# Kernel optimization log

Measured on AMD Instinct MI355X. Metric: run time of the kernel, lower is better.

## Reference

```python
import jax, jax.numpy as jnp
import numpy as np

B, T, F, H = 2048, 512, 64, 16


def setup_inputs() -> dict:
    key = jax.random.key(0)
    ks = jax.random.split(key, 10)
    s = 0.05  # small init so relu-activated LSTM state stays bounded over 512 steps
    return {
        "x": jax.random.normal(ks[0], (B, T, F), dtype=jnp.float32),
        "Wx": jax.random.normal(ks[1], (F, 4 * H), dtype=jnp.float32) * s,
        "Wh": jax.random.normal(ks[2], (H, 4 * H), dtype=jnp.float32) * s,
        "b": jnp.zeros((4 * H,), dtype=jnp.float32),
        "W2": jax.random.normal(ks[3], (H, 8), dtype=jnp.float32) * 0.3,
        "b2": jnp.zeros((8,), dtype=jnp.float32),
        "W3": jax.random.normal(ks[4], (8, 4), dtype=jnp.float32) * 0.3,
        "b3": jnp.zeros((4,), dtype=jnp.float32),
        "Wo": jax.random.normal(ks[5], (4, 1), dtype=jnp.float32) * 0.3,
        "bo": jnp.zeros((1,), dtype=jnp.float32),
    }


def reference(x, Wx, Wh, b, W2, b2, W3, b3, Wo, bo):
    # Keras LSTM, gate order [i, f, c(g), o]; recurrent_activation=sigmoid,
    # activation=relu (applied to candidate g AND to cell state in h = o*relu(c)).
    # Precompute input projections for all timesteps, scan only the recurrence.
    xz = jnp.einsum('btf,fg->btg', x, Wx) + b  # [B, T, 4H]
    h0 = jnp.zeros((x.shape[0], H), dtype=x.dtype)
    c0 = jnp.zeros((x.shape[0], H), dtype=x.dtype)

    def step(carry, xz_t):
        h, c = carry
        z = xz_t + h @ Wh  # [B, 4H]
        i = jax.nn.sigmoid(z[:, 0 * H:1 * H])
        f = jax.nn.sigmoid(z[:, 1 * H:2 * H])
        g = jax.nn.relu(z[:, 2 * H:3 * H])
        o = jax.nn.sigmoid(z[:, 3 * H:4 * H])
        c_new = f * c + i * g
        h_new = o * jax.nn.relu(c_new)
        return (h_new, c_new), None

    (h_T, _), _ = jax.lax.scan(step, (h0, c0), jnp.swapaxes(xz, 0, 1))
    # Dropout layers are identity at inference (training=False).
    x2 = jax.nn.relu(h_T @ W2 + b2)
    x3 = jax.nn.relu(x2 @ W3 + b3)
    return jax.nn.sigmoid(x3 @ Wo + bo)  # [B, 1]
```

## Files before the change

### kernel.cpp

```cpp
#include <hip/hip_runtime.h>
#include <stdint.h>

#define Bdim 2048
#define Tdim 512
#define NTILE 32

typedef __attribute__((ext_vector_type(8))) short bf16x8;
typedef __attribute__((ext_vector_type(4))) float f32x4;

union U32x4 { uint32_t u[4]; bf16x8 v; };

__device__ __forceinline__ uint16_t f2bf(float f) {
    union { float f; uint32_t u; } v; v.f = f;
    uint32_t r = v.u + 0x7fffu + ((v.u >> 16) & 1u);
    return (uint16_t)(r >> 16);
}
__device__ __forceinline__ float sigmoidf(float z) {
    return __builtin_amdgcn_rcpf(1.0f + __expf(-z));
}
__device__ __forceinline__ float fast_exp2(float x) {
#if __has_builtin(__builtin_amdgcn_exp2f)
    return __builtin_amdgcn_exp2f(x);
#else
    return exp2f(x);
#endif
}

#define RORI(M, dst, src)                                                     \
    dst = __builtin_amdgcn_update_dpp((src), (src), 0x120 | (M), 0xF, 0xF, 0)

#define FMAC_ROR(M, ACC)                                                      \
    asm("v_fmac_f32 %0, %1, %2 row_ror:" #M " row_mask:0xf bank_mask:0xf"     \
        : "+v"(ACC) : "v"(h), "v"(w[M]))

__global__ __launch_bounds__(64, 2) void lstm_fused(
    const float* __restrict__ x, const float* __restrict__ Wx,
    const float* __restrict__ bias, const float* __restrict__ Wh,
    const float* __restrict__ W2, const float* __restrict__ b2,
    const float* __restrict__ W3, const float* __restrict__ b3,
    const float* __restrict__ Wo, const float* __restrict__ bo,
    float* __restrict__ out)
{
    __shared__ __align__(16) float zbuf[2048];
    __shared__ float hs[16];

    const int lane = threadIdx.x;
    const int u    = lane & 15;
    const int quad = lane >> 4;
    const int col  = quad * 16 + u;
    const int b    = blockIdx.x;
    const float NL2E = -1.4426950408889634f;
    const float sg   = (quad == 2) ? 1.0f : NL2E;

    float w[16];
    w[0] = Wh[(size_t)u * 64 + col] * sg;
#define WL(M) { int ii_; RORI(M, ii_, u); w[M] = Wh[(size_t)ii_ * 64 + col] * sg; }
    WL(1)  WL(2)  WL(3)  WL(4)  WL(5)  WL(6)  WL(7)
    WL(8)  WL(9)  WL(10) WL(11) WL(12) WL(13) WL(14) WL(15)
#undef WL

    const int adr_i = (u +  0) * 4;
    const int adr_f = (u + 16) * 4;
    const int adr_g = (u + 32) * 4;
    const int adr_o = (u + 48) * 4;

    bf16x8 wxf[4][2];
    float bv[4];
    #pragma unroll
    for (int nt = 0; nt < 4; ++nt) {
        const float s = (nt == 2) ? 1.0f : NL2E;
        #pragma unroll
        for (int kc = 0; kc < 2; ++kc)
            #pragma unroll
            for (int e = 0; e < 8; ++e)
                wxf[nt][kc][e] = (short)f2bf(
                    Wx[(size_t)(kc * 32 + quad * 8 + e) * 64 + nt * 16 + u] * s);
        bv[nt] = bias[nt * 16 + u] * s;
    }

    f32x4 xa0[4], xa1[4];
    auto xload = [&](int tile, f32x4 (&xs)[4]) {
        const float* p = x + ((size_t)b * Tdim + tile * 16 + u) * 64 + quad * 8;
        xs[0] = *(const f32x4*)(p);
        xs[1] = *(const f32x4*)(p + 4);
        xs[2] = *(const f32x4*)(p + 32);
        xs[3] = *(const f32x4*)(p + 36);
    };

    auto proj = [&](const f32x4 (&xs)[4], int buf) {
        U32x4 af[2];
        #pragma unroll
        for (int kc = 0; kc < 2; ++kc) {
            asm("v_cvt_pk_bf16_f32 %0, %1, %2" : "=v"(af[kc].u[0]) : "v"(xs[2*kc][0]),   "v"(xs[2*kc][1]));
            asm("v_cvt_pk_bf16_f32 %0, %1, %2" : "=v"(af[kc].u[1]) : "v"(xs[2*kc][2]),   "v"(xs[2*kc][3]));
            asm("v_cvt_pk_bf16_f32 %0, %1, %2" : "=v"(af[kc].u[2]) : "v"(xs[2*kc+1][0]), "v"(xs[2*kc+1][1]));
            asm("v_cvt_pk_bf16_f32 %0, %1, %2" : "=v"(af[kc].u[3]) : "v"(xs[2*kc+1][2]), "v"(xs[2*kc+1][3]));
        }
        float* zb = zbuf + buf * 1024 + quad * 256 + u * 4;
        #pragma unroll
        for (int nt = 0; nt < 4; ++nt) {
            f32x4 a = {bv[nt], bv[nt], bv[nt], bv[nt]};
            a = __builtin_amdgcn_mfma_f32_16x16x32_bf16(af[0].v, wxf[nt][0], a, 0, 0, 0);
            a = __builtin_amdgcn_mfma_f32_16x16x32_bf16(af[1].v, wxf[nt][1], a, 0, 0, 0);
            *(f32x4*)(zb + nt * 64) = a;
        }
    };

    xload(0, xa0);
    proj(xa0, 0);
    xload(1, xa1);

    float c = 0.f, h = 0.f;
    f32x4 zgA = *(const f32x4*)(zbuf + col * 4);
    f32x4 zgB;

    const bool isrelu = (quad == 2);

    auto scan_tile = [&](int n) {
        const float* curp = zbuf + (n & 1) * 1024 + col * 4;
        const float* othp = zbuf + ((n & 1) ^ 1) * 1024 + col * 4;
        #pragma unroll
        for (int t = 0; t < 16; ++t) {
            const int gl = t >> 2;
            if ((t & 3) == 0) {
                const float* zp = (gl < 3) ? (curp + (gl + 1) * 256) : othp;
                f32x4 zv = *(const f32x4*)zp;
                if (gl & 1) zgA = zv; else zgB = zv;
            }
            const float zval = (gl & 1) ? zgB[t & 3] : zgA[t & 3];

            asm volatile("s_nop 1" : "+v"(h));

            float acc0 = fmaf(h, w[0], zval);
            float acc1 = 0.f;
            FMAC_ROR(1,  acc1); FMAC_ROR(2,  acc0); FMAC_ROR(3,  acc1);
            FMAC_ROR(4,  acc0); FMAC_ROR(5,  acc1); FMAC_ROR(6,  acc0);
            FMAC_ROR(7,  acc1); FMAC_ROR(8,  acc0); FMAC_ROR(9,  acc1);
            FMAC_ROR(10, acc0); FMAC_ROR(11, acc1); FMAC_ROR(12, acc0);
            FMAC_ROR(13, acc1); FMAC_ROR(14, acc0); FMAC_ROR(15, acc1);
            const float zacc = acc0 + acc1;

            const float sig = __builtin_amdgcn_rcpf(1.0f + fast_exp2(zacc));
            const float a   = isrelu ? fmaxf(zacc, 0.0f) : sig;

            const int ia = __float_as_int(a);
            const float gi = __int_as_float(__builtin_amdgcn_ds_bpermute(adr_i, ia));
            const float gf = __int_as_float(__builtin_amdgcn_ds_bpermute(adr_f, ia));
            const float gG = __int_as_float(__builtin_amdgcn_ds_bpermute(adr_g, ia));
            const float go = __int_as_float(__builtin_amdgcn_ds_bpermute(adr_o, ia));

            c = fmaf(gf, c, gi * gG);
            h = go * fmaxf(c, 0.0f);
        }
    };

    #pragma unroll 1
    for (int nn = 0; nn < NTILE / 2; ++nn) {
        {
            const int n = 2 * nn;
            if (n + 2 < NTILE) xload(n + 2, xa0);
            proj(xa1, 1);
            scan_tile(n);
        }
        {
            const int n = 2 * nn + 1;
            if (n + 2 < NTILE) xload(n + 2, xa1);
            if (n + 1 < NTILE) proj(xa0, 0);
            scan_tile(n);
        }
    }

    if (lane < 16) hs[lane] = h;
    if (lane == 0) {
        float x2[8];
        #pragma unroll
        for (int k = 0; k < 8; ++k) {
            float s = b2[k];
            #pragma unroll
            for (int q = 0; q < 16; ++q) s = fmaf(hs[q], W2[(size_t)q * 8 + k], s);
            x2[k] = fmaxf(s, 0.f);
        }
        float x3[4];
        #pragma unroll
        for (int m = 0; m < 4; ++m) {
            float s = b3[m];
            #pragma unroll
            for (int k = 0; k < 8; ++k) s = fmaf(x2[k], W3[(size_t)k * 4 + m], s);
            x3[m] = fmaxf(s, 0.f);
        }
        float s = bo[0];
        #pragma unroll
        for (int m = 0; m < 4; ++m) s = fmaf(x3[m], Wo[m], s);
        out[b] = sigmoidf(s);
    }
}

extern "C" void kernel_launch(void* const* d_in, const int* in_sizes, int n_in,
                              void* d_out, int out_size, void* d_ws, size_t ws_size,
                              hipStream_t stream) {
    const float* x  = (const float*)d_in[0];
    const float* Wx = (const float*)d_in[1];
    const float* Wh = (const float*)d_in[2];
    const float* bb = (const float*)d_in[3];
    const float* W2 = (const float*)d_in[4];
    const float* b2 = (const float*)d_in[5];
    const float* W3 = (const float*)d_in[6];
    const float* b3 = (const float*)d_in[7];
    const float* Wo = (const float*)d_in[8];
    const float* bo = (const float*)d_in[9];

    lstm_fused<<<Bdim, 64, 0, stream>>>(x, Wx, bb, Wh, W2, b2, W3, b3,
                                        Wo, bo, (float*)d_out);
}
```

Measured before the change: 381.2 us.

## Pack four batch rows per wavefront and compute all gates per lane

Each 64-lane wavefront now handles four batch rows (one per 16-lane row group) instead of one, with each lane computing all four gate dot products for its hidden unit. This removes the four ds_bpermute gate exchanges per step, and the grid shrinks to a quarter of the blocks. The cost is four times the DPP FMAs per step, 64 recurrent weights per lane, larger LDS buffers and occupancy hint 1, so the serial per-step latency grows while the work per lane is used better.

```diff
diff --git a/kernel.cpp b/kernel.cpp
--- a/kernel.cpp
+++ b/kernel.cpp
@@ -4,6 +4,7 @@
 #define Bdim 2048
 #define Tdim 512
 #define NTILE 32
+#define ROWS 4
 
 typedef __attribute__((ext_vector_type(8))) short bf16x8;
 typedef __attribute__((ext_vector_type(4))) float f32x4;
@@ -29,11 +30,11 @@
 #define RORI(M, dst, src)                                                     \
     dst = __builtin_amdgcn_update_dpp((src), (src), 0x120 | (M), 0xF, 0xF, 0)
 
-#define FMAC_ROR(M, ACC)                                                      \
+#define FMAC_ROR(M, ACC, H, W)                                                \
     asm("v_fmac_f32 %0, %1, %2 row_ror:" #M " row_mask:0xf bank_mask:0xf"     \
-        : "+v"(ACC) : "v"(h), "v"(w[M]))
-
-__global__ __launch_bounds__(64, 2) void lstm_fused(
+        : "+v"(ACC) : "v"(H), "v"(W))
+
+__global__ __launch_bounds__(64, 1) void lstm_fused(
     const float* __restrict__ x, const float* __restrict__ Wx,
     const float* __restrict__ bias, const float* __restrict__ Wh,
     const float* __restrict__ W2, const float* __restrict__ b2,
@@ -41,28 +42,29 @@
     const float* __restrict__ Wo, const float* __restrict__ bo,
     float* __restrict__ out)
 {
-    __shared__ __align__(16) float zbuf[2048];
-    __shared__ float hs[16];
+    __shared__ __align__(16) float zbuf[8192];
+    __shared__ float hb[64];
 
     const int lane = threadIdx.x;
     const int u    = lane & 15;
     const int quad = lane >> 4;
-    const int col  = quad * 16 + u;
-    const int b    = blockIdx.x;
+    const int b0   = blockIdx.x * ROWS;
     const float NL2E = -1.4426950408889634f;
-    const float sg   = (quad == 2) ? 1.0f : NL2E;
-
-    float w[16];
-    w[0] = Wh[(size_t)u * 64 + col] * sg;
-#define WL(M) { int ii_; RORI(M, ii_, u); w[M] = Wh[(size_t)ii_ * 64 + col] * sg; }
-    WL(1)  WL(2)  WL(3)  WL(4)  WL(5)  WL(6)  WL(7)
-    WL(8)  WL(9)  WL(10) WL(11) WL(12) WL(13) WL(14) WL(15)
-#undef WL
-
-    const int adr_i = (u +  0) * 4;
-    const int adr_f = (u + 16) * 4;
-    const int adr_g = (u + 32) * 4;
-    const int adr_o = (u + 48) * 4;
+
+    int idx[16];
+    idx[0] = u;
+#define PR(M) RORI(M, idx[M], u);
+    PR(1)  PR(2)  PR(3)  PR(4)  PR(5)  PR(6)  PR(7)
+    PR(8)  PR(9)  PR(10) PR(11) PR(12) PR(13) PR(14) PR(15)
+#undef PR
+    float w[4][16];
+    #pragma unroll
+    for (int g = 0; g < 4; ++g) {
+        const float s = (g == 2) ? 1.0f : NL2E;
+        #pragma unroll
+        for (int k = 0; k < 16; ++k)
+            w[g][k] = Wh[(size_t)idx[k] * 64 + g * 16 + u] * s;
+    }
 
     bf16x8 wxf[4][2];
     float bv[4];
@@ -78,106 +80,108 @@
         bv[nt] = bias[nt * 16 + u] * s;
     }
 
-    f32x4 xa0[4], xa1[4];
-    auto xload = [&](int tile, f32x4 (&xs)[4]) {
-        const float* p = x + ((size_t)b * Tdim + tile * 16 + u) * 64 + quad * 8;
-        xs[0] = *(const f32x4*)(p);
-        xs[1] = *(const f32x4*)(p + 4);
-        xs[2] = *(const f32x4*)(p + 32);
-        xs[3] = *(const f32x4*)(p + 36);
+    f32x4 xa[ROWS][4];
+    auto xload = [&](int tile) {
+        #pragma unroll
+        for (int rs = 0; rs < ROWS; ++rs) {
+            const float* p = x + ((size_t)(b0 + rs) * Tdim + tile * 16 + u) * 64
+                               + quad * 8;
+            xa[rs][0] = *(const f32x4*)(p);
+            xa[rs][1] = *(const f32x4*)(p + 4);
+            xa[rs][2] = *(const f32x4*)(p + 32);
+            xa[rs][3] = *(const f32x4*)(p + 36);
+        }
     };
 
-    auto proj = [&](const f32x4 (&xs)[4], int buf) {
-        U32x4 af[2];
-        #pragma unroll
-        for (int kc = 0; kc < 2; ++kc) {
-            asm("v_cvt_pk_bf16_f32 %0, %1, %2" : "=v"(af[kc].u[0]) : "v"(xs[2*kc][0]),   "v"(xs[2*kc][1]));
-            asm("v_cvt_pk_bf16_f32 %0, %1, %2" : "=v"(af[kc].u[1]) : "v"(xs[2*kc][2]),   "v"(xs[2*kc][3]));
-            asm("v_cvt_pk_bf16_f32 %0, %1, %2" : "=v"(af[kc].u[2]) : "v"(xs[2*kc+1][0]), "v"(xs[2*kc+1][1]));
-            asm("v_cvt_pk_bf16_f32 %0, %1, %2" : "=v"(af[kc].u[3]) : "v"(xs[2*kc+1][2]), "v"(xs[2*kc+1][3]));
-        }
-        float* zb = zbuf + buf * 1024 + quad * 256 + u * 4;
-        #pragma unroll
-        for (int nt = 0; nt < 4; ++nt) {
-            f32x4 a = {bv[nt], bv[nt], bv[nt], bv[nt]};
-            a = __builtin_amdgcn_mfma_f32_16x16x32_bf16(af[0].v, wxf[nt][0], a, 0, 0, 0);
-            a = __builtin_amdgcn_mfma_f32_16x16x32_bf16(af[1].v, wxf[nt][1], a, 0, 0, 0);
-            *(f32x4*)(zb + nt * 64) = a;
+    auto proj = [&](int buf) {
+        #pragma unroll
+        for (int rs = 0; rs < ROWS; ++rs) {
+            U32x4 af0, af1;
+            asm("v_cvt_pk_bf16_f32 %0, %1, %2" : "=v"(af0.u[0]) : "v"(xa[rs][0][0]), "v"(xa[rs][0][1]));
+            asm("v_cvt_pk_bf16_f32 %0, %1, %2" : "=v"(af0.u[1]) : "v"(xa[rs][0][2]), "v"(xa[rs][0][3]));
+            asm("v_cvt_pk_bf16_f32 %0, %1, %2" : "=v"(af0.u[2]) : "v"(xa[rs][1][0]), "v"(xa[rs][1][1]));
+            asm("v_cvt_pk_bf16_f32 %0, %1, %2" : "=v"(af0.u[3]) : "v"(xa[rs][1][2]), "v"(xa[rs][1][3]));
+            asm("v_cvt_pk_bf16_f32 %0, %1, %2" : "=v"(af1.u[0]) : "v"(xa[rs][2][0]), "v"(xa[rs][2][1]));
+            asm("v_cvt_pk_bf16_f32 %0, %1, %2" : "=v"(af1.u[1]) : "v"(xa[rs][2][2]), "v"(xa[rs][2][3]));
+            asm("v_cvt_pk_bf16_f32 %0, %1, %2" : "=v"(af1.u[2]) : "v"(xa[rs][3][0]), "v"(xa[rs][3][1]));
+            asm("v_cvt_pk_bf16_f32 %0, %1, %2" : "=v"(af1.u[3]) : "v"(xa[rs][3][2]), "v"(xa[rs][3][3]));
+            f32x4 a0 = {bv[0], bv[0], bv[0], bv[0]};
+            f32x4 a1 = {bv[1], bv[1], bv[1], bv[1]};
+            f32x4 a2 = {bv[2], bv[2], bv[2], bv[2]};
+            f32x4 a3 = {bv[3], bv[3], bv[3], bv[3]};
+            a0 = __builtin_amdgcn_mfma_f32_16x16x32_bf16(af0.v, wxf[0][0], a0, 0, 0, 0);
+            a0 = __builtin_amdgcn_mfma_f32_16x16x32_bf16(af1.v, wxf[0][1], a0, 0, 0, 0);
+            a1 = __builtin_amdgcn_mfma_f32_16x16x32_bf16(af0.v, wxf[1][0], a1, 0, 0, 0);
+            a1 = __builtin_amdgcn_mfma_f32_16x16x32_bf16(af1.v, wxf[1][1], a1, 0, 0, 0);
+            a2 = __builtin_amdgcn_mfma_f32_16x16x32_bf16(af0.v, wxf[2][0], a2, 0, 0, 0);
+            a2 = __builtin_amdgcn_mfma_f32_16x16x32_bf16(af1.v, wxf[2][1], a2, 0, 0, 0);
+            a3 = __builtin_amdgcn_mfma_f32_16x16x32_bf16(af0.v, wxf[3][0], a3, 0, 0, 0);
+            a3 = __builtin_amdgcn_mfma_f32_16x16x32_bf16(af1.v, wxf[3][1], a3, 0, 0, 0);
+            float* zb = zbuf + buf * 4096 + quad * 1024 + rs * 64 + u * 4;
+            #pragma unroll
+            for (int r = 0; r < 4; ++r) {
+                float4 w4;
+                w4.x = a0[r]; w4.y = a1[r]; w4.z = a2[r]; w4.w = a3[r];
+                *(float4*)(zb + r * 256) = w4;
+            }
         }
     };
 
-    xload(0, xa0);
-    proj(xa0, 0);
-    xload(1, xa1);
+    xload(0);
+    proj(0);
+    xload(1);
 
     float c = 0.f, h = 0.f;
-    f32x4 zgA = *(const f32x4*)(zbuf + col * 4);
-    f32x4 zgB;
-
-    const bool isrelu = (quad == 2);
+    f32x4 zc = *(const f32x4*)(zbuf + quad * 64 + u * 4);
 
     auto scan_tile = [&](int n) {
-        const float* curp = zbuf + (n & 1) * 1024 + col * 4;
-        const float* othp = zbuf + ((n & 1) ^ 1) * 1024 + col * 4;
+        const float* zp = zbuf + (n & 1) * 4096 + quad * 64 + u * 4;
+        const float* zo = zbuf + ((n & 1) ^ 1) * 4096 + quad * 64 + u * 4;
         #pragma unroll
         for (int t = 0; t < 16; ++t) {
-            const int gl = t >> 2;
-            if ((t & 3) == 0) {
-                const float* zp = (gl < 3) ? (curp + (gl + 1) * 256) : othp;
-                f32x4 zv = *(const f32x4*)zp;
-                if (gl & 1) zgA = zv; else zgB = zv;
-            }
-            const float zval = (gl & 1) ? zgB[t & 3] : zgA[t & 3];
+            const float* zq = (t < 15) ? (zp + (t + 1) * 256) : zo;
+            f32x4 zn = *(const f32x4*)zq;
 
             asm volatile("s_nop 1" : "+v"(h));
 
-            float acc0 = fmaf(h, w[0], zval);
-            float acc1 = 0.f;
-            FMAC_ROR(1,  acc1); FMAC_ROR(2,  acc0); FMAC_ROR(3,  acc1);
-            FMAC_ROR(4,  acc0); FMAC_ROR(5,  acc1); FMAC_ROR(6,  acc0);
-            FMAC_ROR(7,  acc1); FMAC_ROR(8,  acc0); FMAC_ROR(9,  acc1);
-            FMAC_ROR(10, acc0); FMAC_ROR(11, acc1); FMAC_ROR(12, acc0);
-            FMAC_ROR(13, acc1); FMAC_ROR(14, acc0); FMAC_ROR(15, acc1);
-            const float zacc = acc0 + acc1;
-
-            const float sig = __builtin_amdgcn_rcpf(1.0f + fast_exp2(zacc));
-            const float a   = isrelu ? fmaxf(zacc, 0.0f) : sig;
-
-            const int ia = __float_as_int(a);
-            const float gi = __int_as_float(__builtin_amdgcn_ds_bpermute(adr_i, ia));
-            const float gf = __int_as_float(__builtin_amdgcn_ds_bpermute(adr_f, ia));
-            const float gG = __int_as_float(__builtin_amdgcn_ds_bpermute(adr_g, ia));
-            const float go = __int_as_float(__builtin_amdgcn_ds_bpermute(adr_o, ia));
-
-            c = fmaf(gf, c, gi * gG);
-            h = go * fmaxf(c, 0.0f);
+            float ai = fmaf(h, w[0][0], zc[0]);
+            float afv = fmaf(h, w[1][0], zc[1]);
+            float ag = fmaf(h, w[2][0], zc[2]);
+            float ao = fmaf(h, w[3][0], zc[3]);
+#define DOT4(M) FMAC_ROR(M, ai, h, w[0][M]); FMAC_ROR(M, afv, h, w[1][M]);    \
+                FMAC_ROR(M, ag, h, w[2][M]); FMAC_ROR(M, ao, h, w[3][M]);
+            DOT4(1)  DOT4(2)  DOT4(3)  DOT4(4)  DOT4(5)  DOT4(6)  DOT4(7)
+            DOT4(8)  DOT4(9)  DOT4(10) DOT4(11) DOT4(12) DOT4(13) DOT4(14)
+            DOT4(15)
+#undef DOT4
+
+            const float si = __builtin_amdgcn_rcpf(1.0f + fast_exp2(ai));
+            const float sf = __builtin_amdgcn_rcpf(1.0f + fast_exp2(afv));
+            const float so = __builtin_amdgcn_rcpf(1.0f + fast_exp2(ao));
+            const float gg = fmaxf(ag, 0.0f);
+
+            c = fmaf(sf, c, si * gg);
+            h = so * fmaxf(c, 0.0f);
+            zc = zn;
         }
     };
 
     #pragma unroll 1
-    for (int nn = 0; nn < NTILE / 2; ++nn) {
-        {
-            const int n = 2 * nn;
-            if (n + 2 < NTILE) xload(n + 2, xa0);
-            proj(xa1, 1);
-            scan_tile(n);
-        }
-        {
-            const int n = 2 * nn + 1;
-            if (n + 2 < NTILE) xload(n + 2, xa1);
-            if (n + 1 < NTILE) proj(xa0, 0);
-            scan_tile(n);
-        }
-    }
-
-    if (lane < 16) hs[lane] = h;
-    if (lane == 0) {
+    for (int n = 0; n < NTILE; ++n) {
+        if (n + 1 < NTILE) proj((n + 1) & 1);
+        if (n + 2 < NTILE) xload(n + 2);
+        scan_tile(n);
+    }
+
+    hb[quad * 16 + u] = h;
+    if (lane < ROWS) {
+        const float* hp = &hb[lane * 16];
         float x2[8];
         #pragma unroll
         for (int k = 0; k < 8; ++k) {
             float s = b2[k];
             #pragma unroll
-            for (int q = 0; q < 16; ++q) s = fmaf(hs[q], W2[(size_t)q * 8 + k], s);
+            for (int q = 0; q < 16; ++q) s = fmaf(hp[q], W2[(size_t)q * 8 + k], s);
             x2[k] = fmaxf(s, 0.f);
         }
         float x3[4];
@@ -191,7 +195,7 @@
         float s = bo[0];
         #pragma unroll
         for (int m = 0; m < 4; ++m) s = fmaf(x3[m], Wo[m], s);
-        out[b] = sigmoidf(s);
+        out[b0 + lane] = sigmoidf(s);
     }
 }
 
@@ -209,6 +213,6 @@
     const float* Wo = (const float*)d_in[8];
     const float* bo = (const float*)d_in[9];
 
-    lstm_fused<<<Bdim, 64, 0, stream>>>(x, Wx, bb, Wh, W2, b2, W3, b3,
-                                        Wo, bo, (float*)d_out);
-}
+    lstm_fused<<<Bdim / ROWS, 64, 0, stream>>>(x, Wx, bb, Wh, W2, b2, W3, b3,
+                                               Wo, bo, (float*)d_out);
+}
```

Result: slower. 398.1 us (+4.4%).
